# Optimization experiments

Measured on AMD Instinct MI355X. Metric: run time of the kernel, lower is better.

## Reference

```python
import jax, jax.numpy as jnp
import numpy as np

HEAD_DIM = 32
KERNEL = 3
DILATION = 2


def _unfold(x, k, dil):
    """torch.nn.Unfold with stride=1, padding=dil*(k-1)//2.
    x: [B, C, H, W] -> patches [B, C, k*k, H, W] (kernel positions row-major,
    channel-major overall, matching torch's (B, C*k*k, L) layout)."""
    B, C, H, W = x.shape
    pad = dil * (k - 1) // 2
    xp = jnp.pad(x, ((0, 0), (0, 0), (pad, pad), (pad, pad)))
    patches = jnp.stack(
        [xp[:, :, i * dil:i * dil + H, j * dil:j * dil + W]
         for i in range(k) for j in range(k)],
        axis=2,
    )
    return patches  # [B, C, k*k, H, W]


def setup_inputs() -> dict:
    key = jax.random.key(0)
    kq, kk, kv = jax.random.split(key, 3)
    shape = (8, 384, 56, 56)
    return {
        "q": jax.random.normal(kq, shape, dtype=jnp.float32),
        "k": jax.random.normal(kk, shape, dtype=jnp.float32),
        "v": jax.random.normal(kv, shape, dtype=jnp.float32),
    }


def reference(q, k, v):
    B, d, H, W = q.shape
    h = d // HEAD_DIM
    N = H * W
    k2 = KERNEL * KERNEL
    scale = HEAD_DIM ** (-0.5)

    # q: [B, h, N, hd]
    qr = q.reshape(B, h, HEAD_DIM, N).transpose(0, 1, 3, 2)
    # k patches: [B, h, hd, k2, N]
    kp = _unfold(k, KERNEL, DILATION).reshape(B, h, HEAD_DIM, k2, N)
    attn = jnp.einsum('bhnd,bhdkn->bhnk', qr, kp) * scale
    attn = jax.nn.softmax(attn, axis=-1)
    # v patches: [B, h, hd, k2, N]
    vp = _unfold(v, KERNEL, DILATION).reshape(B, h, HEAD_DIM, k2, N)
    out = jnp.einsum('bhnk,bhdkn->bhnd', attn, vp)  # [B, h, N, hd]
    # transpose(1,2) then reshape(B, H, W, d)
    return out.transpose(0, 2, 1, 3).reshape(B, H, W, d)
```

## Files before the change

### kernel.cpp

```cpp
#include <hip/hip_runtime.h>

#define HD 32
#define NHEADS 12
#define HH 56
#define WW 56
#define NN (HH * WW)
#define BB 8
#define CC (HD * NHEADS)
#define QCH 8
#define TILE 128
#define SCALE 0.17677669529663689f

__global__ __launch_bounds__(256) void dilate_attn_kernel(
    const float* __restrict__ q,
    const float* __restrict__ k,
    const float* __restrict__ v,
    float* __restrict__ out)
{
    const int tx = threadIdx.x;
    const int qc = threadIdx.y;
    const int n0 = blockIdx.x * TILE + 2 * tx;
    const int bh = blockIdx.y;
    const int b = bh / NHEADS;
    const int head = bh - b * NHEADS;
    const bool active = (n0 < NN);

    const int y = n0 / WW;
    const int x0 = n0 - y * WW;
    const bool xlo = (x0 == 0);
    const bool xhi = (x0 == WW - 2);

    const int base0 = (b * CC + head * HD + qc * QCH) * NN;

    __shared__ float2 part[4][64][9];

    float qv[QCH][2];
    if (active) {
#pragma unroll
        for (int d = 0; d < QCH; ++d) {
            const float2 t = *reinterpret_cast<const float2*>(q + base0 + d * NN + n0);
            qv[d][0] = t.x; qv[d][1] = t.y;
        }
    } else {
#pragma unroll
        for (int d = 0; d < QCH; ++d) { qv[d][0] = 0.f; qv[d][1] = 0.f; }
    }

    float lg[9][2];
#pragma unroll
    for (int t = 0; t < 9; ++t) { lg[t][0] = 0.f; lg[t][1] = 0.f; }

#pragma unroll
    for (int r = 0; r < 3; ++r) {
        const int ny = y + (r - 1) * 2;
        const bool rv = active && ((unsigned)ny < HH);
        const int rowbase = base0 + ny * WW + x0;
#pragma unroll
        for (int d = 0; d < QCH; ++d) {
            const float* kb = k + rowbase + d * NN;
            float2 w0 = make_float2(0.f, 0.f);
            float2 w1 = make_float2(0.f, 0.f);
            float2 w2 = make_float2(0.f, 0.f);
            if (rv) {
                w1 = *reinterpret_cast<const float2*>(kb);
                if (!xlo) w0 = *reinterpret_cast<const float2*>(kb - 2);
                if (!xhi) w2 = *reinterpret_cast<const float2*>(kb + 2);
            }
            lg[r * 3 + 0][0] = fmaf(qv[d][0], w0.x, lg[r * 3 + 0][0]);
            lg[r * 3 + 0][1] = fmaf(qv[d][1], w0.y, lg[r * 3 + 0][1]);
            lg[r * 3 + 1][0] = fmaf(qv[d][0], w1.x, lg[r * 3 + 1][0]);
            lg[r * 3 + 1][1] = fmaf(qv[d][1], w1.y, lg[r * 3 + 1][1]);
            lg[r * 3 + 2][0] = fmaf(qv[d][0], w2.x, lg[r * 3 + 2][0]);
            lg[r * 3 + 2][1] = fmaf(qv[d][1], w2.y, lg[r * 3 + 2][1]);
        }
    }

#pragma unroll
    for (int t = 0; t < 9; ++t) part[qc][tx][t] = make_float2(lg[t][0], lg[t][1]);
    __syncthreads();
#pragma unroll
    for (int o = 1; o < 4; ++o) {
        const int oq = (qc + o) & 3;
#pragma unroll
        for (int t = 0; t < 9; ++t) {
            const float2 p = part[oq][tx][t];
            lg[t][0] += p.x; lg[t][1] += p.y;
        }
    }

#pragma unroll
    for (int j = 0; j < 2; ++j) {
        float m = lg[0][j] * SCALE;
#pragma unroll
        for (int t = 0; t < 9; ++t) { lg[t][j] *= SCALE; m = fmaxf(m, lg[t][j]); }
        float s = 0.f;
#pragma unroll
        for (int t = 0; t < 9; ++t) { const float e = __expf(lg[t][j] - m); lg[t][j] = e; s += e; }
        const float inv = 1.f / s;
#pragma unroll
        for (int t = 0; t < 9; ++t) lg[t][j] *= inv;
    }

    float acc[QCH][2];
#pragma unroll
    for (int d = 0; d < QCH; ++d) { acc[d][0] = 0.f; acc[d][1] = 0.f; }

#pragma unroll
    for (int r = 0; r < 3; ++r) {
        const int ny = y + (r - 1) * 2;
        const bool rv = active && ((unsigned)ny < HH);
        const int rowbase = base0 + ny * WW + x0;
#pragma unroll
        for (int d = 0; d < QCH; ++d) {
            const float* vb = v + rowbase + d * NN;
            float2 w0 = make_float2(0.f, 0.f);
            float2 w1 = make_float2(0.f, 0.f);
            float2 w2 = make_float2(0.f, 0.f);
            if (rv) {
                w1 = *reinterpret_cast<const float2*>(vb);
                if (!xlo) w0 = *reinterpret_cast<const float2*>(vb - 2);
                if (!xhi) w2 = *reinterpret_cast<const float2*>(vb + 2);
            }
            acc[d][0] = fmaf(lg[r * 3 + 0][0], w0.x, acc[d][0]);
            acc[d][1] = fmaf(lg[r * 3 + 0][1], w0.y, acc[d][1]);
            acc[d][0] = fmaf(lg[r * 3 + 1][0], w1.x, acc[d][0]);
            acc[d][1] = fmaf(lg[r * 3 + 1][1], w1.y, acc[d][1]);
            acc[d][0] = fmaf(lg[r * 3 + 2][0], w2.x, acc[d][0]);
            acc[d][1] = fmaf(lg[r * 3 + 2][1], w2.y, acc[d][1]);
        }
    }

    if (active) {
#pragma unroll
        for (int j = 0; j < 2; ++j) {
            float* ob = out + ((b * HH + y) * WW + (x0 + j)) * CC + head * HD + qc * QCH;
            *reinterpret_cast<float4*>(ob)     = make_float4(acc[0][j], acc[1][j], acc[2][j], acc[3][j]);
            *reinterpret_cast<float4*>(ob + 4) = make_float4(acc[4][j], acc[5][j], acc[6][j], acc[7][j]);
        }
    }
}

extern "C" void kernel_launch(void* const* d_in, const int* in_sizes, int n_in,
                              void* d_out, int out_size, void* d_ws, size_t ws_size,
                              hipStream_t stream) {
    const float* q = (const float*)d_in[0];
    const float* k = (const float*)d_in[1];
    const float* v = (const float*)d_in[2];
    float* out = (float*)d_out;

    dim3 block(64, 4);
    dim3 grid((NN + TILE - 1) / TILE, BB * NHEADS);
    dilate_attn_kernel<<<grid, block, 0, stream>>>(q, k, v, out);
}
```

Before: 186.0 us.

## Split head channels across 8 lanes with shuffle reduction and branchless masked loads

Each pixel pair is now handled by 8 lanes that each own 4 channels, and the partial logits are reduced with wave shuffles instead of a shared-memory exchange and a block barrier. Boundary handling switches from predicated loads to clamped addresses plus multiplicative masks, so every load is issued unconditionally. The grid is sized exactly (49 blocks of 32 pairs), which removes the inactive-thread checks. Writes per thread shrink to one float4 per pixel, and global access along each channel becomes more strided within a wave, which may hurt coalescing.

Result: slower. 274.6 us (+47.6%).

```diff
diff --git a/kernel.cpp b/kernel.cpp
--- a/kernel.cpp
+++ b/kernel.cpp
@@ -7,8 +7,6 @@
 #define NN (HH * WW)
 #define BB 8
 #define CC (HD * NHEADS)
-#define QCH 8
-#define TILE 128
 #define SCALE 0.17677669529663689f
 
 __global__ __launch_bounds__(256) void dilate_attn_kernel(
@@ -17,74 +15,66 @@
     const float* __restrict__ v,
     float* __restrict__ out)
 {
-    const int tx = threadIdx.x;
-    const int qc = threadIdx.y;
-    const int n0 = blockIdx.x * TILE + 2 * tx;
-    const int bh = blockIdx.y;
-    const int b = bh / NHEADS;
+    const int lane = threadIdx.x & 63;
+    const int wid  = threadIdx.x >> 6;
+    const int cg   = lane & 7;
+    const int pr   = lane >> 3;
+    const int pair = (blockIdx.x * 4 + wid) * 8 + pr;
+    const int n0   = 2 * pair;
+    const int bh   = blockIdx.y;
+    const int b    = bh / NHEADS;
     const int head = bh - b * NHEADS;
-    const bool active = (n0 < NN);
 
-    const int y = n0 / WW;
+    const int y  = n0 / WW;
     const int x0 = n0 - y * WW;
-    const bool xlo = (x0 == 0);
-    const bool xhi = (x0 == WW - 2);
+    const float mlo = (x0 == 0)      ? 0.f : 1.f;
+    const float mhi = (x0 == WW - 2) ? 0.f : 1.f;
+    const int offlo = (x0 == 0)      ? 0 : -2;
+    const int offhi = (x0 == WW - 2) ? 0 :  2;
 
-    const int base0 = (b * CC + head * HD + qc * QCH) * NN;
+    const int base0 = (b * CC + head * HD + cg * 4) * NN;
 
-    __shared__ float2 part[4][64][9];
-
-    float qv[QCH][2];
-    if (active) {
+    float qv[4][2];
 #pragma unroll
-        for (int d = 0; d < QCH; ++d) {
-            const float2 t = *reinterpret_cast<const float2*>(q + base0 + d * NN + n0);
-            qv[d][0] = t.x; qv[d][1] = t.y;
-        }
-    } else {
-#pragma unroll
-        for (int d = 0; d < QCH; ++d) { qv[d][0] = 0.f; qv[d][1] = 0.f; }
+    for (int d = 0; d < 4; ++d) {
+        const float2 t = *reinterpret_cast<const float2*>(q + base0 + d * NN + n0);
+        qv[d][0] = t.x; qv[d][1] = t.y;
     }
 
     float lg[9][2];
-#pragma unroll
-    for (int t = 0; t < 9; ++t) { lg[t][0] = 0.f; lg[t][1] = 0.f; }
-
+    float rm[3];
 #pragma unroll
     for (int r = 0; r < 3; ++r) {
         const int ny = y + (r - 1) * 2;
-        const bool rv = active && ((unsigned)ny < HH);
-        const int rowbase = base0 + ny * WW + x0;
+        rm[r] = ((unsigned)ny < HH) ? 1.f : 0.f;
+        const int nyc = ny < 0 ? 0 : (ny > HH - 1 ? HH - 1 : ny);
+        const int rowbase = base0 + nyc * WW + x0;
+        float s0x = 0.f, s0y = 0.f, s1x = 0.f, s1y = 0.f, s2x = 0.f, s2y = 0.f;
 #pragma unroll
-        for (int d = 0; d < QCH; ++d) {
+        for (int d = 0; d < 4; ++d) {
             const float* kb = k + rowbase + d * NN;
-            float2 w0 = make_float2(0.f, 0.f);
-            float2 w1 = make_float2(0.f, 0.f);
-            float2 w2 = make_float2(0.f, 0.f);
-            if (rv) {
-                w1 = *reinterpret_cast<const float2*>(kb);
-                if (!xlo) w0 = *reinterpret_cast<const float2*>(kb - 2);
-                if (!xhi) w2 = *reinterpret_cast<const float2*>(kb + 2);
-            }
-            lg[r * 3 + 0][0] = fmaf(qv[d][0], w0.x, lg[r * 3 + 0][0]);
-            lg[r * 3 + 0][1] = fmaf(qv[d][1], w0.y, lg[r * 3 + 0][1]);
-            lg[r * 3 + 1][0] = fmaf(qv[d][0], w1.x, lg[r * 3 + 1][0]);
-            lg[r * 3 + 1][1] = fmaf(qv[d][1], w1.y, lg[r * 3 + 1][1]);
-            lg[r * 3 + 2][0] = fmaf(qv[d][0], w2.x, lg[r * 3 + 2][0]);
-            lg[r * 3 + 2][1] = fmaf(qv[d][1], w2.y, lg[r * 3 + 2][1]);
+            const float2 w0 = *reinterpret_cast<const float2*>(kb + offlo);
+            const float2 w1 = *reinterpret_cast<const float2*>(kb);
+            const float2 w2 = *reinterpret_cast<const float2*>(kb + offhi);
+            s0x = fmaf(qv[d][0], w0.x, s0x); s0y = fmaf(qv[d][1], w0.y, s0y);
+            s1x = fmaf(qv[d][0], w1.x, s1x); s1y = fmaf(qv[d][1], w1.y, s1y);
+            s2x = fmaf(qv[d][0], w2.x, s2x); s2y = fmaf(qv[d][1], w2.y, s2y);
         }
+        const float m0 = rm[r] * mlo, m2 = rm[r] * mhi;
+        lg[r * 3 + 0][0] = s0x * m0;    lg[r * 3 + 0][1] = s0y * m0;
+        lg[r * 3 + 1][0] = s1x * rm[r]; lg[r * 3 + 1][1] = s1y * rm[r];
+        lg[r * 3 + 2][0] = s2x * m2;    lg[r * 3 + 2][1] = s2y * m2;
     }
 
 #pragma unroll
-    for (int t = 0; t < 9; ++t) part[qc][tx][t] = make_float2(lg[t][0], lg[t][1]);
-    __syncthreads();
+    for (int t = 0; t < 9; ++t) {
 #pragma unroll
-    for (int o = 1; o < 4; ++o) {
-        const int oq = (qc + o) & 3;
-#pragma unroll
-        for (int t = 0; t < 9; ++t) {
-            const float2 p = part[oq][tx][t];
-            lg[t][0] += p.x; lg[t][1] += p.y;
+        for (int j = 0; j < 2; ++j) {
+            float s = lg[t][j];
+            s += __shfl_xor(s, 1);
+            s += __shfl_xor(s, 2);
+            s += __shfl_xor(s, 4);
+            lg[t][j] = s;
         }
     }
 
@@ -100,43 +90,41 @@
 #pragma unroll
         for (int t = 0; t < 9; ++t) lg[t][j] *= inv;
     }
+#pragma unroll
+    for (int r = 0; r < 3; ++r) {
+        lg[r * 3 + 0][0] *= rm[r] * mlo; lg[r * 3 + 0][1] *= rm[r] * mlo;
+        lg[r * 3 + 1][0] *= rm[r];       lg[r * 3 + 1][1] *= rm[r];
+        lg[r * 3 + 2][0] *= rm[r] * mhi; lg[r * 3 + 2][1] *= rm[r] * mhi;
+    }
 
-    float acc[QCH][2];
+    float acc[4][2];
 #pragma unroll
-    for (int d = 0; d < QCH; ++d) { acc[d][0] = 0.f; acc[d][1] = 0.f; }
-
+    for (int d = 0; d < 4; ++d) { acc[d][0] = 0.f; acc[d][1] = 0.f; }
 #pragma unroll
     for (int r = 0; r < 3; ++r) {
         const int ny = y + (r - 1) * 2;
-        const bool rv = active && ((unsigned)ny < HH);
-        const int rowbase = base0 + ny * WW + x0;
+        const int nyc = ny < 0 ? 0 : (ny > HH - 1 ? HH - 1 : ny);
+        const int rowbase = base0 + nyc * WW + x0;
+        const float w0x = lg[r * 3 + 0][0], w0y = lg[r * 3 + 0][1];
+        const float w1x = lg[r * 3 + 1][0], w1y = lg[r * 3 + 1][1];
+        const float w2x = lg[r * 3 + 2][0], w2y = lg[r * 3 + 2][1];
 #pragma unroll
-        for (int d = 0; d < QCH; ++d) {
+        for (int d = 0; d < 4; ++d) {
             const float* vb = v + rowbase + d * NN;
-            float2 w0 = make_float2(0.f, 0.f);
-            float2 w1 = make_float2(0.f, 0.f);
-            float2 w2 = make_float2(0.f, 0.f);
-            if (rv) {
-                w1 = *reinterpret_cast<const float2*>(vb);
-                if (!xlo) w0 = *reinterpret_cast<const float2*>(vb - 2);
-                if (!xhi) w2 = *reinterpret_cast<const float2*>(vb + 2);
-            }
-            acc[d][0] = fmaf(lg[r * 3 + 0][0], w0.x, acc[d][0]);
-            acc[d][1] = fmaf(lg[r * 3 + 0][1], w0.y, acc[d][1]);
-            acc[d][0] = fmaf(lg[r * 3 + 1][0], w1.x, acc[d][0]);
-            acc[d][1] = fmaf(lg[r * 3 + 1][1], w1.y, acc[d][1]);
-            acc[d][0] = fmaf(lg[r * 3 + 2][0], w2.x, acc[d][0]);
-            acc[d][1] = fmaf(lg[r * 3 + 2][1], w2.y, acc[d][1]);
+            const float2 u0 = *reinterpret_cast<const float2*>(vb + offlo);
+            const float2 u1 = *reinterpret_cast<const float2*>(vb);
+            const float2 u2 = *reinterpret_cast<const float2*>(vb + offhi);
+            acc[d][0] = fmaf(w0x, u0.x, acc[d][0]); acc[d][1] = fmaf(w0y, u0.y, acc[d][1]);
+            acc[d][0] = fmaf(w1x, u1.x, acc[d][0]); acc[d][1] = fmaf(w1y, u1.y, acc[d][1]);
+            acc[d][0] = fmaf(w2x, u2.x, acc[d][0]); acc[d][1] = fmaf(w2y, u2.y, acc[d][1]);
         }
     }
 
-    if (active) {
 #pragma unroll
-        for (int j = 0; j < 2; ++j) {
-            float* ob = out + ((b * HH + y) * WW + (x0 + j)) * CC + head * HD + qc * QCH;
-            *reinterpret_cast<float4*>(ob)     = make_float4(acc[0][j], acc[1][j], acc[2][j], acc[3][j]);
-            *reinterpret_cast<float4*>(ob + 4) = make_float4(acc[4][j], acc[5][j], acc[6][j], acc[7][j]);
-        }
+    for (int j = 0; j < 2; ++j) {
+        float* ob = out + ((b * HH + y) * WW + (x0 + j)) * CC + head * HD + cg * 4;
+        *reinterpret_cast<float4*>(ob) =
+            make_float4(acc[0][j], acc[1][j], acc[2][j], acc[3][j]);
     }
 }
 
@@ -148,7 +136,7 @@
     const float* v = (const float*)d_in[2];
     float* out = (float*)d_out;
 
-    dim3 block(64, 4);
-    dim3 grid((NN + TILE - 1) / TILE, BB * NHEADS);
+    dim3 block(256);
+    dim3 grid(49, BB * NHEADS);
     dilate_attn_kernel<<<grid, block, 0, stream>>>(q, k, v, out);
 }
```

## Share neighbor columns via wave shuffles and prefetch all K/V rows upfront

Applied to the files above, without the earlier changes.

Each block now covers exactly two image rows (112 pixels), so a 64-lane wavefront holds whole rows. The horizontal neighbors at ±2 columns are taken from adjacent lanes with __shfl_up/__shfl_down instead of separate global loads, cutting K/V load instructions roughly threefold. Out-of-range rows are clamped, and boundary taps are zeroed with multiplicative masks in place of branches. All 24 K and 24 V float2 values are loaded at the start to raise memory-level parallelism. In exchange, 8 of every 64 lanes sit idle, register pressure goes up, and there are extra shuffle instructions.

Result: faster. 165.6 us (-10.9%).

```diff
diff --git a/kernel.cpp b/kernel.cpp
--- a/kernel.cpp
+++ b/kernel.cpp
@@ -7,8 +7,6 @@
 #define NN (HH * WW)
 #define BB 8
 #define CC (HD * NHEADS)
-#define QCH 8
-#define TILE 128
 #define SCALE 0.17677669529663689f
 
 __global__ __launch_bounds__(256) void dilate_attn_kernel(
@@ -19,60 +17,70 @@
 {
     const int tx = threadIdx.x;
     const int qc = threadIdx.y;
-    const int n0 = blockIdx.x * TILE + 2 * tx;
     const int bh = blockIdx.y;
     const int b = bh / NHEADS;
     const int head = bh - b * NHEADS;
-    const bool active = (n0 < NN);
 
-    const int y = n0 / WW;
+    const int n0r = blockIdx.x * 112 + 2 * tx;
+    const int n0 = (n0r <= NN - 2) ? n0r : NN - 2;
+    const bool active = (tx < 56);
+
+    const int y  = n0 / WW;
     const int x0 = n0 - y * WW;
-    const bool xlo = (x0 == 0);
-    const bool xhi = (x0 == WW - 2);
+    const float mlo = (x0 == 0)      ? 0.f : 1.f;
+    const float mhi = (x0 == WW - 2) ? 0.f : 1.f;
 
-    const int base0 = (b * CC + head * HD + qc * QCH) * NN;
+    const int base0 = (b * CC + head * HD + qc * 8) * NN;
 
     __shared__ float2 part[4][64][9];
 
-    float qv[QCH][2];
-    if (active) {
+    float2 qv[8];
 #pragma unroll
-        for (int d = 0; d < QCH; ++d) {
-            const float2 t = *reinterpret_cast<const float2*>(q + base0 + d * NN + n0);
-            qv[d][0] = t.x; qv[d][1] = t.y;
-        }
-    } else {
+    for (int d = 0; d < 8; ++d)
+        qv[d] = *reinterpret_cast<const float2*>(q + base0 + d * NN + n0);
+
+    float rm[3]; int rb[3];
 #pragma unroll
-        for (int d = 0; d < QCH; ++d) { qv[d][0] = 0.f; qv[d][1] = 0.f; }
+    for (int r = 0; r < 3; ++r) {
+        const int ny = y + (r - 1) * 2;
+        rm[r] = ((unsigned)ny < HH) ? 1.f : 0.f;
+        const int nyc = ny < 0 ? 0 : (ny > HH - 1 ? HH - 1 : ny);
+        rb[r] = base0 + nyc * WW + x0;
     }
+
+    float2 km[3][8];
+#pragma unroll
+    for (int r = 0; r < 3; ++r)
+#pragma unroll
+        for (int d = 0; d < 8; ++d)
+            km[r][d] = *reinterpret_cast<const float2*>(k + rb[r] + d * NN);
+
+    float2 vm[3][8];
+#pragma unroll
+    for (int r = 0; r < 3; ++r)
+#pragma unroll
+        for (int d = 0; d < 8; ++d)
+            vm[r][d] = *reinterpret_cast<const float2*>(v + rb[r] + d * NN);
 
     float lg[9][2];
 #pragma unroll
-    for (int t = 0; t < 9; ++t) { lg[t][0] = 0.f; lg[t][1] = 0.f; }
-
+    for (int r = 0; r < 3; ++r) {
+        float s0x = 0.f, s0y = 0.f, s1x = 0.f, s1y = 0.f, s2x = 0.f, s2y = 0.f;
 #pragma unroll
-    for (int r = 0; r < 3; ++r) {
-        const int ny = y + (r - 1) * 2;
-        const bool rv = active && ((unsigned)ny < HH);
-        const int rowbase = base0 + ny * WW + x0;
-#pragma unroll
-        for (int d = 0; d < QCH; ++d) {
-            const float* kb = k + rowbase + d * NN;
-            float2 w0 = make_float2(0.f, 0.f);
-            float2 w1 = make_float2(0.f, 0.f);
-            float2 w2 = make_float2(0.f, 0.f);
-            if (rv) {
-                w1 = *reinterpret_cast<const float2*>(kb);
-                if (!xlo) w0 = *reinterpret_cast<const float2*>(kb - 2);
-                if (!xhi) w2 = *reinterpret_cast<const float2*>(kb + 2);
-            }
-            lg[r * 3 + 0][0] = fmaf(qv[d][0], w0.x, lg[r * 3 + 0][0]);
-            lg[r * 3 + 0][1] = fmaf(qv[d][1], w0.y, lg[r * 3 + 0][1]);
-            lg[r * 3 + 1][0] = fmaf(qv[d][0], w1.x, lg[r * 3 + 1][0]);
-            lg[r * 3 + 1][1] = fmaf(qv[d][1], w1.y, lg[r * 3 + 1][1]);
-            lg[r * 3 + 2][0] = fmaf(qv[d][0], w2.x, lg[r * 3 + 2][0]);
-            lg[r * 3 + 2][1] = fmaf(qv[d][1], w2.y, lg[r * 3 + 2][1]);
+        for (int d = 0; d < 8; ++d) {
+            const float2 w1 = km[r][d];
+            const float w0x = __shfl_up(w1.x, 1);
+            const float w0y = __shfl_up(w1.y, 1);
+            const float w2x = __shfl_down(w1.x, 1);
+            const float w2y = __shfl_down(w1.y, 1);
+            s0x = fmaf(qv[d].x, w0x, s0x);  s0y = fmaf(qv[d].y, w0y, s0y);
+            s1x = fmaf(qv[d].x, w1.x, s1x); s1y = fmaf(qv[d].y, w1.y, s1y);
+            s2x = fmaf(qv[d].x, w2x, s2x);  s2y = fmaf(qv[d].y, w2y, s2y);
         }
+        const float m0 = rm[r] * mlo, m2 = rm[r] * mhi;
+        lg[r * 3 + 0][0] = s0x * m0;    lg[r * 3 + 0][1] = s0y * m0;
+        lg[r * 3 + 1][0] = s1x * rm[r]; lg[r * 3 + 1][1] = s1y * rm[r];
+        lg[r * 3 + 2][0] = s2x * m2;    lg[r * 3 + 2][1] = s2y * m2;
     }
 
 #pragma unroll
@@ -100,40 +108,39 @@
 #pragma unroll
         for (int t = 0; t < 9; ++t) lg[t][j] *= inv;
     }
-
-    float acc[QCH][2];
-#pragma unroll
-    for (int d = 0; d < QCH; ++d) { acc[d][0] = 0.f; acc[d][1] = 0.f; }
-
 #pragma unroll
     for (int r = 0; r < 3; ++r) {
-        const int ny = y + (r - 1) * 2;
-        const bool rv = active && ((unsigned)ny < HH);
-        const int rowbase = base0 + ny * WW + x0;
+        const float m0 = rm[r] * mlo, m2 = rm[r] * mhi;
+        lg[r * 3 + 0][0] *= m0;    lg[r * 3 + 0][1] *= m0;
+        lg[r * 3 + 1][0] *= rm[r]; lg[r * 3 + 1][1] *= rm[r];
+        lg[r * 3 + 2][0] *= m2;    lg[r * 3 + 2][1] *= m2;
+    }
+
+    float acc[8][2];
 #pragma unroll
-        for (int d = 0; d < QCH; ++d) {
-            const float* vb = v + rowbase + d * NN;
-            float2 w0 = make_float2(0.f, 0.f);
-            float2 w1 = make_float2(0.f, 0.f);
-            float2 w2 = make_float2(0.f, 0.f);
-            if (rv) {
-                w1 = *reinterpret_cast<const float2*>(vb);
-                if (!xlo) w0 = *reinterpret_cast<const float2*>(vb - 2);
-                if (!xhi) w2 = *reinterpret_cast<const float2*>(vb + 2);
-            }
-            acc[d][0] = fmaf(lg[r * 3 + 0][0], w0.x, acc[d][0]);
-            acc[d][1] = fmaf(lg[r * 3 + 0][1], w0.y, acc[d][1]);
-            acc[d][0] = fmaf(lg[r * 3 + 1][0], w1.x, acc[d][0]);
-            acc[d][1] = fmaf(lg[r * 3 + 1][1], w1.y, acc[d][1]);
-            acc[d][0] = fmaf(lg[r * 3 + 2][0], w2.x, acc[d][0]);
-            acc[d][1] = fmaf(lg[r * 3 + 2][1], w2.y, acc[d][1]);
+    for (int d = 0; d < 8; ++d) { acc[d][0] = 0.f; acc[d][1] = 0.f; }
+#pragma unroll
+    for (int r = 0; r < 3; ++r) {
+        const float g0x = lg[r * 3 + 0][0], g0y = lg[r * 3 + 0][1];
+        const float g1x = lg[r * 3 + 1][0], g1y = lg[r * 3 + 1][1];
+        const float g2x = lg[r * 3 + 2][0], g2y = lg[r * 3 + 2][1];
+#pragma unroll
+        for (int d = 0; d < 8; ++d) {
+            const float2 u1 = vm[r][d];
+            const float u0x = __shfl_up(u1.x, 1);
+            const float u0y = __shfl_up(u1.y, 1);
+            const float u2x = __shfl_down(u1.x, 1);
+            const float u2y = __shfl_down(u1.y, 1);
+            acc[d][0] = fmaf(g0x, u0x, acc[d][0]);  acc[d][1] = fmaf(g0y, u0y, acc[d][1]);
+            acc[d][0] = fmaf(g1x, u1.x, acc[d][0]); acc[d][1] = fmaf(g1y, u1.y, acc[d][1]);
+            acc[d][0] = fmaf(g2x, u2x, acc[d][0]);  acc[d][1] = fmaf(g2y, u2y, acc[d][1]);
         }
     }
 
     if (active) {
 #pragma unroll
         for (int j = 0; j < 2; ++j) {
-            float* ob = out + ((b * HH + y) * WW + (x0 + j)) * CC + head * HD + qc * QCH;
+            float* ob = out + ((b * HH + y) * WW + (x0 + j)) * CC + head * HD + qc * 8;
             *reinterpret_cast<float4*>(ob)     = make_float4(acc[0][j], acc[1][j], acc[2][j], acc[3][j]);
             *reinterpret_cast<float4*>(ob + 4) = make_float4(acc[4][j], acc[5][j], acc[6][j], acc[7][j]);
         }
@@ -149,6 +156,6 @@
     float* out = (float*)d_out;
 
     dim3 block(64, 4);
-    dim3 grid((NN + TILE - 1) / TILE, BB * NHEADS);
+    dim3 grid(NN / 112, BB * NHEADS);
     dilate_attn_kernel<<<grid, block, 0, stream>>>(q, k, v, out);
 }
```
